# Kernel optimization log

Hardware: AMD Instinct MI355X
Metric: run time of the kernel (lower is better)

The kernel has to match this reference:

```python
import jax, jax.numpy as jnp
import numpy as np

HEADS = 6


def setup_inputs() -> dict:
    key = jax.random.key(0)
    ks = jax.random.split(key, 4)
    B, N, C = 4, 1024, 384
    s = 0.02
    return {
        "x": jax.random.normal(ks[0], (B, N, C), jnp.float32),
        "qkv_w": jax.random.normal(ks[1], (C, 3 * C), jnp.float32) * s,  # (in, out) layout
        "qkv_b": jnp.zeros((3 * C,), jnp.float32),
        "proj_w": jax.random.normal(ks[2], (C, C), jnp.float32) * s,
        "proj_b": jnp.zeros((C,), jnp.float32),
        "conv_w": jax.random.normal(ks[3], (HEADS, HEADS), jnp.float32) * s,  # 1x1 conv kernel (out_ch, in_ch)
        "conv_b": jnp.zeros((HEADS,), jnp.float32),
    }


def _forward(x, qkv_w, qkv_b, proj_w, proj_b, conv_w, conv_b):
    B, N, C = x.shape
    H = HEADS
    D = C // H
    scale = D ** -0.5
    qkv = (x @ qkv_w + qkv_b).reshape(B, N, 3, H, D)
    q = jnp.transpose(qkv[:, :, 0], (0, 2, 1, 3))  # bhnd
    k = jnp.transpose(qkv[:, :, 1], (0, 2, 1, 3))
    v = jnp.transpose(qkv[:, :, 2], (0, 2, 1, 3))
    qk = jnp.einsum('bhnd,bhmd->bhnm', q, k)          # raw scores (pre-scale)
    attn_mean = jax.nn.softmax(qk * scale, axis=-1)
    # data_uncertainty: 1x1 conv mixing the head channels of qk
    u = jnp.einsum('oh,bhnm->bonm', conv_w, qk) + conv_b[None, :, None, None]
    # norm_uncertainty: log(exp(u)) == u (kept faithful), then (tanh+1)/2
    u = jnp.log(jnp.exp(u))
    u = (jnp.tanh(u) + 1.0) * 0.5
    # gumbel-softmax (hard, tau=1) over logits [u, 1-u]; channel 1 selected.
    # softmax over 2 classes == sigmoid of logit difference; hard == argmax.
    gk = jax.random.key(42)
    g0 = jax.random.gumbel(jax.random.fold_in(gk, 0), u.shape, u.dtype)
    g1 = jax.random.gumbel(jax.random.fold_in(gk, 1), u.shape, u.dtype)
    l0 = u + g0
    l1 = (1.0 - u) + g1
    soft1 = jax.nn.sigmoid(l1 - l0)
    hard1 = (l1 > l0).astype(u.dtype)
    mask = hard1 + soft1 - jax.lax.stop_gradient(soft1)  # straight-through estimator
    attn = attn_mean * mask  # attn_drop is identity in eval / dropout=0
    out = jnp.einsum('bhnm,bhmd->bnhd', attn, v).reshape(B, N, C)
    out = out @ proj_w + proj_b  # proj_drop identity
    return out, attn_mean, u


def reference(x, qkv_w, qkv_b, proj_w, proj_b, conv_w, conv_b):
    return _forward(x, qkv_w, qkv_b, proj_w, proj_b, conv_w, conv_b)
```

## Files before the change

### kernel.cpp

```cpp
#include <hip/hip_runtime.h>
#include <hip/hip_bf16.h>
#include <stdint.h>
#include <stddef.h>

#define B_ 4
#define N_ 1024
#define C_ 384
#define H_ 6
#define D_ 64
#define TC_ 1152
#define BHNN_ 25165824
#define SCALE 0.125f
#define LOG2E 1.4426950408889634f
#define LN2 0.6931471805599453f

typedef __hip_bfloat16 bf16;
typedef __attribute__((ext_vector_type(2))) float f32x2;
typedef __attribute__((ext_vector_type(4))) float f32x4;
typedef __attribute__((ext_vector_type(8))) short short8;
typedef __attribute__((ext_vector_type(4))) short short4v;

union f4u { f32x4 v4; f32x2 v2[2]; };

__device__ __forceinline__ short f2bs(float x){
  bf16 b = __float2bfloat16(x);
  return *reinterpret_cast<short*>(&b);
}

__device__ __forceinline__ void pk_fma_ll(f32x2& c, f32x2 a, f32x2 b){
  asm("v_pk_fma_f32 %0, %1, %2, %0 op_sel:[0,0,0] op_sel_hi:[0,1,1]" : "+v"(c) : "v"(a), "v"(b));
}
__device__ __forceinline__ void pk_fma_hh(f32x2& c, f32x2 a, f32x2 b){
  asm("v_pk_fma_f32 %0, %1, %2, %0 op_sel:[1,0,0] op_sel_hi:[1,1,1]" : "+v"(c) : "v"(a), "v"(b));
}

#define TFR(x0,x1,r) { x0 += x1; x1 = ((x1)<<(r))|((x1)>>(32-(r))); x1 ^= x0; }

__host__ __device__ __forceinline__ void tf2x32(uint32_t k0, uint32_t k1,
                                                uint32_t& x0, uint32_t& x1){
  uint32_t k2 = k0 ^ k1 ^ 0x1BD11BDAu;
  x0 += k0; x1 += k1;
  TFR(x0,x1,13) TFR(x0,x1,15) TFR(x0,x1,26) TFR(x0,x1,6)
  x0 += k1; x1 += k2 + 1u;
  TFR(x0,x1,17) TFR(x0,x1,29) TFR(x0,x1,16) TFR(x0,x1,24)
  x0 += k2; x1 += k0 + 2u;
  TFR(x0,x1,13) TFR(x0,x1,15) TFR(x0,x1,26) TFR(x0,x1,6)
  x0 += k0; x1 += k1 + 3u;
  TFR(x0,x1,17) TFR(x0,x1,29) TFR(x0,x1,16) TFR(x0,x1,24)
  x0 += k1; x1 += k2 + 4u;
  TFR(x0,x1,13) TFR(x0,x1,15) TFR(x0,x1,26) TFR(x0,x1,6)
  x0 += k2; x1 += k0 + 5u;
}

__device__ __forceinline__ uint32_t rotl32(uint32_t x, uint32_t r){
#if __has_builtin(__builtin_amdgcn_alignbit)
  return __builtin_amdgcn_alignbit(x, x, 32u - r);
#else
  return (x << r) | (x >> (32u - r));
#endif
}

__device__ __forceinline__ void tf_dual(uint32_t j,
    uint32_t ak0, uint32_t ak1, uint32_t ak2,
    uint32_t bk0, uint32_t bk1, uint32_t bk2,
    float& fA, float& fB){
  uint32_t x0 = ak0, x1 = j + ak1;
  uint32_t y0 = bk0, y1 = j + bk1;
  #define DTFR(r) { x0 += x1; y0 += y1;               \
                    x1 = rotl32(x1,(r)); y1 = rotl32(y1,(r)); \
                    x1 ^= x0; y1 ^= y0; }
  DTFR(13) DTFR(15) DTFR(26) DTFR(6)
  x0 += ak1; x1 += ak2 + 1u;  y0 += bk1; y1 += bk2 + 1u;
  DTFR(17) DTFR(29) DTFR(16) DTFR(24)
  x0 += ak2; x1 += ak0 + 2u;  y0 += bk2; y1 += bk0 + 2u;
  DTFR(13) DTFR(15) DTFR(26) DTFR(6)
  x0 += ak0; x1 += ak1 + 3u;  y0 += bk0; y1 += bk1 + 3u;
  DTFR(17) DTFR(29) DTFR(16) DTFR(24)
  x0 += ak1; x1 += ak2 + 4u;  y0 += bk1; y1 += bk2 + 4u;
  DTFR(13) DTFR(15) DTFR(26) DTFR(6)
  x0 += ak2; x1 += ak0 + 5u;  y0 += bk2; y1 += bk0 + 5u;
  #undef DTFR
  uint32_t bitsA = x0 ^ x1;
  uint32_t bitsB = y0 ^ y1;
  fA = fmaxf(__uint_as_float((bitsA >> 9) | 0x3F800000u) - 1.0f, 1.1754943508222875e-38f);
  fB = fmaxf(__uint_as_float((bitsB >> 9) | 0x3F800000u) - 1.0f, 1.1754943508222875e-38f);
}

__global__ __launch_bounds__(256) void k_prep(const float* __restrict__ x,
                                              const float* __restrict__ w,
                                              short* __restrict__ xhi, short* __restrict__ xlo,
                                              short* __restrict__ wThi, short* __restrict__ wTlo){
  const int t = threadIdx.x;
  if (blockIdx.x < 432){
    const int kt = blockIdx.x % 12, nt = blockIdx.x / 12;
    __shared__ float T[32][33];
    const int col = t & 31, row8 = t >> 5;
    #pragma unroll
    for (int i = 0; i < 4; i++)
      T[row8 + i*8][col] = w[(size_t)(kt*32 + row8 + i*8)*TC_ + nt*32 + col];
    __syncthreads();
    #pragma unroll
    for (int i = 0; i < 4; i++){
      int n = nt*32 + row8 + i*8;
      int k = kt*32 + col;
      float v = T[col][row8 + i*8];
      bf16 hb = __float2bfloat16(v);
      float hf = __bfloat162float(hb);
      bf16 lb = __float2bfloat16(v - hf);
      wThi[(size_t)n*C_ + k] = *(short*)&hb;
      wTlo[(size_t)n*C_ + k] = *(short*)&lb;
    }
  } else {
    const int b2 = blockIdx.x - 432;
    size_t base = ((size_t)b2*256 + t) * 4;
    #pragma unroll
    for (int it = 0; it < 8; it++){
      size_t idx = base + (size_t)it * 196608;
      f32x4 v = *(const f32x4*)&x[idx];
      short4v hs, ls;
      #pragma unroll
      for (int jj = 0; jj < 4; jj++){
        bf16 hb = __float2bfloat16(v[jj]);
        float hf = __bfloat162float(hb);
        bf16 lb = __float2bfloat16(v[jj] - hf);
        hs[jj] = *(short*)&hb; ls[jj] = *(short*)&lb;
      }
      *(short4v*)&xhi[idx] = hs;
      *(short4v*)&xlo[idx] = ls;
    }
  }
}

__global__ __launch_bounds__(256) void k_qkv(const short* __restrict__ xhi,
                                             const short* __restrict__ xlo,
                                             const short* __restrict__ wThi,
                                             const short* __restrict__ wTlo,
                                             const float* __restrict__ bias,
                                             bf16* __restrict__ qb,
                                             bf16* __restrict__ kb,
                                             bf16* __restrict__ vTb){
  __shared__ __align__(16) short sA[2][64][32];
  __shared__ __align__(16) short sB[2][64][32];
  const int t = threadIdx.x, lane = t & 63, wv = t >> 6;
  const int lo = lane & 15, quad = lane >> 4;
  const int m0 = blockIdx.x * 64, n0 = blockIdx.y * 64;
  const int sr = lane >> 2, skq = lane & 3;
  const short* srcAh = xhi  + (size_t)(m0 + wv*16 + sr)*C_ + skq*8;
  const short* srcAl = xlo  + (size_t)(m0 + wv*16 + sr)*C_ + skq*8;
  const short* srcBh = wThi + (size_t)(n0 + wv*16 + sr)*C_ + skq*8;
  const short* srcBl = wTlo + (size_t)(n0 + wv*16 + sr)*C_ + skq*8;
  short* dAh = &sA[0][wv*16 + sr][skq*8];
  short* dAl = &sA[1][wv*16 + sr][skq*8];
  short* dBh = &sB[0][wv*16 + sr][skq*8];
  short* dBl = &sB[1][wv*16 + sr][skq*8];

  f32x4 acc[4] = {{0,0,0,0},{0,0,0,0},{0,0,0,0},{0,0,0,0}};
  short8 ra = *(const short8*)(srcAh);
  short8 rb = *(const short8*)(srcAl);
  short8 rc = *(const short8*)(srcBh);
  short8 rd = *(const short8*)(srcBl);
  for (int k0 = 0; k0 < C_; k0 += 32){
    __syncthreads();
    *(short8*)dAh = ra; *(short8*)dAl = rb;
    *(short8*)dBh = rc; *(short8*)dBl = rd;
    if (k0 + 32 < C_){
      ra = *(const short8*)(srcAh + k0 + 32);
      rb = *(const short8*)(srcAl + k0 + 32);
      rc = *(const short8*)(srcBh + k0 + 32);
      rd = *(const short8*)(srcBl + k0 + 32);
    }
    __syncthreads();
    short8 ah = *(const short8*)&sA[0][wv*16 + lo][quad*8];
    short8 al = *(const short8*)&sA[1][wv*16 + lo][quad*8];
    #pragma unroll
    for (int j = 0; j < 4; j++){
      short8 bh = *(const short8*)&sB[0][j*16 + lo][quad*8];
      short8 bl = *(const short8*)&sB[1][j*16 + lo][quad*8];
      acc[j] = __builtin_amdgcn_mfma_f32_16x16x32_bf16(ah, bh, acc[j], 0, 0, 0);
      acc[j] = __builtin_amdgcn_mfma_f32_16x16x32_bf16(ah, bl, acc[j], 0, 0, 0);
      acc[j] = __builtin_amdgcn_mfma_f32_16x16x32_bf16(al, bh, acc[j], 0, 0, 0);
    }
  }
  #pragma unroll
  for (int j = 0; j < 4; j++){
    int ng = n0 + j*16 + lo;
    int t3 = ng / C_;
    int rem = ng - t3*C_;
    int hh = rem >> 6, dd = rem & 63;
    float bsv = bias[ng];
    #pragma unroll
    for (int r = 0; r < 4; r++){
      int mg = m0 + wv*16 + quad*4 + r;
      int bb = mg >> 10, nn = mg & 1023;
      bf16 val = __float2bfloat16(acc[j][r] + bsv);
      if (t3 == 0)      qb[((size_t)(bb*H_ + hh)*N_ + nn)*D_ + dd] = val;
      else if (t3 == 1) kb[((size_t)(bb*H_ + hh)*N_ + nn)*D_ + dd] = val;
      else              vTb[((size_t)(bb*H_ + hh)*D_ + dd)*N_ + nn] = val;
    }
  }
}

__global__ __launch_bounds__(256) void k_scores(const short* __restrict__ qb,
                                                const short* __restrict__ kb,
                                                float* __restrict__ qk){
  const int gw = blockIdx.x * 4 + (threadIdx.x >> 6);
  const int lane = threadIdx.x & 63;
  const int mt = gw & 63, nt = (gw >> 6) & 63, bh = gw >> 12;
  const int lo = lane & 15, quad = lane >> 4;
  const short* qrow = qb + ((size_t)bh*N_ + nt*16 + lo)*D_ + quad*8;
  const short* krow = kb + ((size_t)bh*N_ + mt*16 + lo)*D_ + quad*8;
  short8 a0 = *(const short8*)qrow;
  short8 b0 = *(const short8*)krow;
  short8 a1 = *(const short8*)(qrow + 32);
  short8 b1 = *(const short8*)(krow + 32);
  f32x4 acc = {0.f, 0.f, 0.f, 0.f};
  acc = __builtin_amdgcn_mfma_f32_16x16x32_bf16(a0, b0, acc, 0, 0, 0);
  acc = __builtin_amdgcn_mfma_f32_16x16x32_bf16(a1, b1, acc, 0, 0, 0);
  float* o = qk + (size_t)bh*N_*N_ + (size_t)(nt*16)*N_ + mt*16;
  #pragma unroll
  for (int r = 0; r < 4; r++)
    o[(size_t)(quad*4 + r)*N_ + lo] = acc[r];
}

__global__ __launch_bounds__(256) void k_fuse(float* __restrict__ attn,
                                              const float* __restrict__ cw,
                                              const float* __restrict__ cb,
                                              float* __restrict__ u_out,
                                              unsigned long long* __restrict__ mbits,
                                              uint32_t g0k0, uint32_t g0k1,
                                              uint32_t g1k0, uint32_t g1k1){
  const int bn = blockIdx.x;
  const int bb = bn >> 10, n = bn & 1023;
  const int t = threadIdx.x, lane = t & 63, wid = t >> 6;
  __shared__ float redm[H_][4], reds[H_][4];

  float qv[H_][4];
  #pragma unroll
  for (int h = 0; h < H_; h++){
    const float* p = attn + (((size_t)(bb*H_ + h) << 10) + n) * N_;
    #pragma unroll
    for (int i = 0; i < 4; i++) qv[h][i] = p[t + 256*i];
  }
  #pragma unroll
  for (int h = 0; h < H_; h++){
    float mx = fmaxf(fmaxf(qv[h][0], qv[h][1]), fmaxf(qv[h][2], qv[h][3]));
    #pragma unroll
    for (int off = 32; off > 0; off >>= 1) mx = fmaxf(mx, __shfl_xor(mx, off));
    if (lane == 0) redm[h][wid] = mx;
  }
  __syncthreads();
  float mxh[H_], sm[H_];
  #pragma unroll
  for (int h = 0; h < H_; h++){
    mxh[h] = fmaxf(fmaxf(redm[h][0], redm[h][1]), fmaxf(redm[h][2], redm[h][3]));
    const float k2 = SCALE * LOG2E;
    float s = 0.f;
    #pragma unroll
    for (int i = 0; i < 4; i++) s += __builtin_amdgcn_exp2f((qv[h][i] - mxh[h]) * k2);
    #pragma unroll
    for (int off = 32; off > 0; off >>= 1) s += __shfl_xor(s, off);
    if (lane == 0) reds[h][wid] = s;
    sm[h] = s;
  }
  __syncthreads();
  float invS[H_];
  #pragma unroll
  for (int h = 0; h < H_; h++){
    float S = reds[h][0] + reds[h][1] + reds[h][2] + reds[h][3];
    invS[h] = __builtin_amdgcn_rcpf(S);
  }
  #pragma unroll
  for (int h = 0; h < H_; h++){
    float* p = attn + (((size_t)(bb*H_ + h) << 10) + n) * N_;
    const float k2 = SCALE * LOG2E;
    #pragma unroll
    for (int i = 0; i < 4; i++)
      p[t + 256*i] = __builtin_amdgcn_exp2f((qv[h][i] - mxh[h]) * k2) * invS[h];
  }
  const uint32_t a2k = g0k0 ^ g0k1 ^ 0x1BD11BDAu;
  const uint32_t b2k = g1k0 ^ g1k1 ^ 0x1BD11BDAu;
  const uint32_t jrow = ((uint32_t)(bb*H_) << 20) | ((uint32_t)n << 10);
  #pragma unroll
  for (int i = 0; i < 4; i++){
    const uint32_t m = (uint32_t)(t + 256*i);
    #pragma unroll
    for (int o = 0; o < H_; o++){
      float up = cb[o];
      #pragma unroll
      for (int h = 0; h < H_; h++) up += cw[o*H_ + h] * qv[h][i];
      float eneg = __builtin_amdgcn_exp2f(-2.0f * LOG2E * up);
      float uu   = __builtin_amdgcn_rcpf(1.0f + eneg);
      float tt   = 2.0f * uu - 1.0f;
      float et   = __builtin_amdgcn_exp2f(tt * LOG2E);
      uint32_t j = jrow + ((uint32_t)o << 20) + m;
      float f0, f1;
      tf_dual(j, g0k0, g0k1, a2k, g1k0, g1k1, b2k, f0, f1);
      float L0 = __builtin_amdgcn_logf(f0);
      float L1 = __builtin_amdgcn_logf(f1);
      int hard = L0 < L1 * et;
      u_out[(size_t)j] = uu;
      unsigned long long bal = __ballot(hard);
      if (lane == 0) mbits[(size_t)j >> 6] = bal;
    }
  }
}

__global__ __launch_bounds__(256) void k_av(const float* __restrict__ attn,
                                            const unsigned long long* __restrict__ mbits,
                                            const short* __restrict__ vTb,
                                            float* __restrict__ tmp){
  __shared__ __align__(16) float red[2][4][64][4];
  const int w = threadIdx.x >> 6, lane = threadIdx.x & 63;
  const int ntl = w >> 1, mh = w & 1;
  const int bh = blockIdx.x >> 5, ntp = blockIdx.x & 31;
  const int nt = ntp*2 + ntl;
  const int bb = bh / H_, h = bh - bb*H_;
  const int lo = lane & 15, quad = lane >> 4;
  const int row = nt*16 + lo;
  const float* arow = attn + ((size_t)bh*N_ + row)*N_ + quad*8;
  const unsigned long long* mrow = mbits + (((size_t)bh*N_ + row)*N_ >> 6);
  const short* vbase = vTb + ((size_t)bh*D_ + lo)*N_ + quad*8;
  f32x4 acc[4] = {{0,0,0,0},{0,0,0,0},{0,0,0,0},{0,0,0,0}};
  const int mstart = mh * 512;
  for (int m0 = mstart; m0 < mstart + 512; m0 += 32){
    f32x4 av0 = *(const f32x4*)(arow + m0);
    f32x4 av1 = *(const f32x4*)(arow + m0 + 4);
    unsigned long long wb = mrow[(m0 + quad*8) >> 6];
    int base = (m0 + quad*8) & 63;
    float vals[8] = {av0[0], av0[1], av0[2], av0[3], av1[0], av1[1], av1[2], av1[3]};
    short8 a;
    #pragma unroll
    for (int j = 0; j < 8; j++)
      a[j] = f2bs(((wb >> (base + j)) & 1ull) ? vals[j] : 0.0f);
    #pragma unroll
    for (int dt = 0; dt < 4; dt++){
      short8 bv = *(const short8*)(vbase + (size_t)(dt*16)*N_ + m0);
      acc[dt] = __builtin_amdgcn_mfma_f32_16x16x32_bf16(a, bv, acc[dt], 0, 0, 0);
    }
  }
  if (mh == 1){
    #pragma unroll
    for (int dt = 0; dt < 4; dt++)
      *(f32x4*)&red[ntl][dt][lane][0] = acc[dt];
  }
  __syncthreads();
  if (mh == 0){
    float* o = tmp + ((size_t)(bb*N_) + nt*16)*C_ + h*D_;
    #pragma unroll
    for (int dt = 0; dt < 4; dt++){
      f32x4 other = *(const f32x4*)&red[ntl][dt][lane][0];
      f32x4 s = acc[dt] + other;
      #pragma unroll
      for (int r = 0; r < 4; r++)
        o[(size_t)(quad*4 + r)*C_ + dt*16 + lo] = s[r];
    }
  }
}

__global__ __launch_bounds__(256) void k_proj(const float* __restrict__ A,
                                              const float* __restrict__ w,
                                              const float* __restrict__ bias,
                                              float* __restrict__ out){
  __shared__ __align__(16) float As[16][36];
  __shared__ __align__(16) float Bs[16][68];
  const int t = threadIdx.x, tx = t & 15, ty = t >> 4;
  const int m0 = blockIdx.x * 32, n0 = blockIdx.y * 64;
  const int am = t >> 3,        ak = (t & 7) * 2;
  const int bn = (t & 15) * 4,  bk = t >> 4;
  f32x2 c[2][2] = {};
  for (int k0 = 0; k0 < C_; k0 += 16){
    f32x2 av = *(const f32x2*)&A[(size_t)(m0+am)*C_ + k0 + ak];
    f32x4 bv = *(const f32x4*)&w[(size_t)(k0+bk)*C_ + n0 + bn];
    __syncthreads();
    As[ak+0][am] = av[0]; As[ak+1][am] = av[1];
    *(f32x4*)&Bs[bk][bn] = bv;
    __syncthreads();
    #pragma unroll
    for (int k = 0; k < 16; k++){
      f32x2 a2 = *(const f32x2*)&As[k][ty*2];
      f4u b; b.v4 = *(const f32x4*)&Bs[k][tx*4];
      pk_fma_ll(c[0][0], a2, b.v2[0]); pk_fma_ll(c[0][1], a2, b.v2[1]);
      pk_fma_hh(c[1][0], a2, b.v2[0]); pk_fma_hh(c[1][1], a2, b.v2[1]);
    }
  }
  #pragma unroll
  for (int i = 0; i < 2; i++)
    #pragma unroll
    for (int jp = 0; jp < 2; jp++)
      #pragma unroll
      for (int sub = 0; sub < 2; sub++){
        int jg = n0 + tx*4 + jp*2 + sub;
        out[(size_t)(m0+ty*2+i)*C_ + jg] = c[i][jp][sub] + bias[jg];
      }
}

extern "C" void kernel_launch(void* const* d_in, const int* in_sizes, int n_in,
                              void* d_out, int out_size, void* d_ws, size_t ws_size,
                              hipStream_t stream) {
  const float* x      = (const float*)d_in[0];
  const float* qkv_w  = (const float*)d_in[1];
  const float* qkv_b  = (const float*)d_in[2];
  const float* proj_w = (const float*)d_in[3];
  const float* proj_b = (const float*)d_in[4];
  const float* conv_w = (const float*)d_in[5];
  const float* conv_b = (const float*)d_in[6];

  float* out      = (float*)d_out;
  float* attn_out = out + (size_t)B_*N_*C_;
  float* u_out    = attn_out + (size_t)BHNN_;

  char* ws = (char*)d_ws;
  bf16*  qb    = (bf16*)ws;
  bf16*  kb    = (bf16*)(ws + 3145728);
  bf16*  vTb   = (bf16*)(ws + 6291456);
  unsigned long long* mbits = (unsigned long long*)(ws + 9437184);
  float* tmp   = (float*)(ws + 12582912);
  short* xhi   = (short*)(ws + 18874368);
  short* xlo   = (short*)(ws + 22020096);
  short* wThi  = (short*)(ws + 25165824);
  short* wTlo  = (short*)(ws + 26050560);

  uint32_t g0k0, g0k1, g1k0, g1k1;
  { uint32_t a = 0u, b = 0u; tf2x32(0u, 42u, a, b); g0k0 = a; g0k1 = b; }
  { uint32_t a = 0u, b = 1u; tf2x32(0u, 42u, a, b); g1k0 = a; g1k1 = b; }

  dim3 blk(256);
  k_prep  <<<dim3(624),     blk, 0, stream>>>(x, qkv_w, xhi, xlo, wThi, wTlo);
  k_qkv   <<<dim3(64, 18),  blk, 0, stream>>>(xhi, xlo, wThi, wTlo, qkv_b, qb, kb, vTb);
  k_scores<<<dim3(24576),   blk, 0, stream>>>((const short*)qb, (const short*)kb, attn_out);
  k_fuse  <<<dim3(4096),    blk, 0, stream>>>(attn_out, conv_w, conv_b,
                                              u_out, mbits,
                                              g0k0, g0k1, g1k0, g1k1);
  k_av    <<<dim3(768),     blk, 0, stream>>>(attn_out, mbits, (const short*)vTb, tmp);
  k_proj  <<<dim3(128, 6),  blk, 0, stream>>>(tmp, proj_w, proj_b, out);
}
```

Before: 436.1 us.

## Write masked bf16 attention in fuse kernel and swizzle GEMM block mapping

When the workspace is large enough, the fuse kernel writes the masked softmax probabilities directly as bf16. A new AV kernel then streams that bf16 matrix instead of re-reading fp32 attention plus mask bits, cutting AV read traffic roughly in half at the cost of an extra 50MB write. The QKV and projection GEMMs also remap their block indices so that blocks spread across XCDs share tiles, aiming for better L2 locality. The active path depends on the runtime workspace size.

```diff
diff --git a/kernel.cpp b/kernel.cpp
--- a/kernel.cpp
+++ b/kernel.cpp
@@ -143,7 +143,8 @@
   __shared__ __align__(16) short sB[2][64][32];
   const int t = threadIdx.x, lane = t & 63, wv = t >> 6;
   const int lo = lane & 15, quad = lane >> 4;
-  const int m0 = blockIdx.x * 64, n0 = blockIdx.y * 64;
+  const int wg = (blockIdx.x & 7) * 144 + (blockIdx.x >> 3);
+  const int m0 = (wg / 18) * 64, n0 = (wg % 18) * 64;
   const int sr = lane >> 2, skq = lane & 3;
   const short* srcAh = xhi  + (size_t)(m0 + wv*16 + sr)*C_ + skq*8;
   const short* srcAl = xlo  + (size_t)(m0 + wv*16 + sr)*C_ + skq*8;
@@ -222,11 +223,13 @@
     o[(size_t)(quad*4 + r)*N_ + lo] = acc[r];
 }
 
-__global__ __launch_bounds__(256) void k_fuse(float* __restrict__ attn,
+template<bool WRITE_AB>
+__global__ __launch_bounds__(256) void k_fuse_t(float* __restrict__ attn,
                                               const float* __restrict__ cw,
                                               const float* __restrict__ cb,
                                               float* __restrict__ u_out,
                                               unsigned long long* __restrict__ mbits,
+                                              bf16* __restrict__ ab,
                                               uint32_t g0k0, uint32_t g0k1,
                                               uint32_t g1k0, uint32_t g1k1){
   const int bn = blockIdx.x;
@@ -249,7 +252,7 @@
     if (lane == 0) redm[h][wid] = mx;
   }
   __syncthreads();
-  float mxh[H_], sm[H_];
+  float mxh[H_];
   #pragma unroll
   for (int h = 0; h < H_; h++){
     mxh[h] = fmaxf(fmaxf(redm[h][0], redm[h][1]), fmaxf(redm[h][2], redm[h][3]));
@@ -260,7 +263,6 @@
     #pragma unroll
     for (int off = 32; off > 0; off >>= 1) s += __shfl_xor(s, off);
     if (lane == 0) reds[h][wid] = s;
-    sm[h] = s;
   }
   __syncthreads();
   float invS[H_];
@@ -299,8 +301,15 @@
       float L1 = __builtin_amdgcn_logf(f1);
       int hard = L0 < L1 * et;
       u_out[(size_t)j] = uu;
-      unsigned long long bal = __ballot(hard);
-      if (lane == 0) mbits[(size_t)j >> 6] = bal;
+      if (WRITE_AB){
+        const float k2 = SCALE * LOG2E;
+        float e = __builtin_amdgcn_exp2f((qv[o][i] - mxh[o]) * k2) * invS[o];
+        bf16 mv = __float2bfloat16(hard ? e : 0.0f);
+        ab[(size_t)j] = mv;
+      } else {
+        unsigned long long bal = __ballot(hard);
+        if (lane == 0) mbits[(size_t)j >> 6] = bal;
+      }
     }
   }
 }
@@ -357,6 +366,48 @@
   }
 }
 
+__global__ __launch_bounds__(256) void k_av2(const short* __restrict__ ab,
+                                             const short* __restrict__ vTb,
+                                             float* __restrict__ tmp){
+  __shared__ __align__(16) float red[2][4][64][4];
+  const int w = threadIdx.x >> 6, lane = threadIdx.x & 63;
+  const int ntl = w >> 1, mh = w & 1;
+  const int bh = blockIdx.x >> 5, ntp = blockIdx.x & 31;
+  const int nt = ntp*2 + ntl;
+  const int bb = bh / H_, h = bh - bb*H_;
+  const int lo = lane & 15, quad = lane >> 4;
+  const int row = nt*16 + lo;
+  const short* abrow = ab + ((size_t)bh*N_ + row)*N_ + quad*8;
+  const short* vbase = vTb + ((size_t)bh*D_ + lo)*N_ + quad*8;
+  f32x4 acc[4] = {{0,0,0,0},{0,0,0,0},{0,0,0,0},{0,0,0,0}};
+  const int mstart = mh * 512;
+  for (int m0 = mstart; m0 < mstart + 512; m0 += 32){
+    short8 a = *(const short8*)(abrow + m0);
+    #pragma unroll
+    for (int dt = 0; dt < 4; dt++){
+      short8 bv = *(const short8*)(vbase + (size_t)(dt*16)*N_ + m0);
+      acc[dt] = __builtin_amdgcn_mfma_f32_16x16x32_bf16(a, bv, acc[dt], 0, 0, 0);
+    }
+  }
+  if (mh == 1){
+    #pragma unroll
+    for (int dt = 0; dt < 4; dt++)
+      *(f32x4*)&red[ntl][dt][lane][0] = acc[dt];
+  }
+  __syncthreads();
+  if (mh == 0){
+    float* o = tmp + ((size_t)(bb*N_) + nt*16)*C_ + h*D_;
+    #pragma unroll
+    for (int dt = 0; dt < 4; dt++){
+      f32x4 other = *(const f32x4*)&red[ntl][dt][lane][0];
+      f32x4 s = acc[dt] + other;
+      #pragma unroll
+      for (int r = 0; r < 4; r++)
+        o[(size_t)(quad*4 + r)*C_ + dt*16 + lo] = s[r];
+    }
+  }
+}
+
 __global__ __launch_bounds__(256) void k_proj(const float* __restrict__ A,
                                               const float* __restrict__ w,
                                               const float* __restrict__ bias,
@@ -364,7 +415,8 @@
   __shared__ __align__(16) float As[16][36];
   __shared__ __align__(16) float Bs[16][68];
   const int t = threadIdx.x, tx = t & 15, ty = t >> 4;
-  const int m0 = blockIdx.x * 32, n0 = blockIdx.y * 64;
+  const int wg = ((int)blockIdx.x & 7) * 96 + ((int)blockIdx.x >> 3);
+  const int m0 = (wg / 6) * 32, n0 = (wg % 6) * 64;
   const int am = t >> 3,        ak = (t & 7) * 2;
   const int bn = (t & 15) * 4,  bk = t >> 4;
   f32x2 c[2][2] = {};
@@ -419,6 +471,8 @@
   short* xlo   = (short*)(ws + 22020096);
   short* wThi  = (short*)(ws + 25165824);
   short* wTlo  = (short*)(ws + 26050560);
+  bf16*  ab    = (bf16*)(ws + 26935296);
+  const bool big_ws = ws_size >= (size_t)77266944;
 
   uint32_t g0k0, g0k1, g1k0, g1k1;
   { uint32_t a = 0u, b = 0u; tf2x32(0u, 42u, a, b); g0k0 = a; g0k1 = b; }
@@ -426,11 +480,18 @@
 
   dim3 blk(256);
   k_prep  <<<dim3(624),     blk, 0, stream>>>(x, qkv_w, xhi, xlo, wThi, wTlo);
-  k_qkv   <<<dim3(64, 18),  blk, 0, stream>>>(xhi, xlo, wThi, wTlo, qkv_b, qb, kb, vTb);
+  k_qkv   <<<dim3(1152),    blk, 0, stream>>>(xhi, xlo, wThi, wTlo, qkv_b, qb, kb, vTb);
   k_scores<<<dim3(24576),   blk, 0, stream>>>((const short*)qb, (const short*)kb, attn_out);
-  k_fuse  <<<dim3(4096),    blk, 0, stream>>>(attn_out, conv_w, conv_b,
-                                              u_out, mbits,
-                                              g0k0, g0k1, g1k0, g1k1);
-  k_av    <<<dim3(768),     blk, 0, stream>>>(attn_out, mbits, (const short*)vTb, tmp);
-  k_proj  <<<dim3(128, 6),  blk, 0, stream>>>(tmp, proj_w, proj_b, out);
-}
+  if (big_ws){
+    k_fuse_t<true> <<<dim3(4096), blk, 0, stream>>>(attn_out, conv_w, conv_b,
+                                                    u_out, mbits, ab,
+                                                    g0k0, g0k1, g1k0, g1k1);
+    k_av2 <<<dim3(768),     blk, 0, stream>>>((const short*)ab, (const short*)vTb, tmp);
+  } else {
+    k_fuse_t<false><<<dim3(4096), blk, 0, stream>>>(attn_out, conv_w, conv_b,
+                                                    u_out, mbits, ab,
+                                                    g0k0, g0k1, g1k0, g1k1);
+    k_av  <<<dim3(768),     blk, 0, stream>>>(attn_out, mbits, (const short*)vTb, tmp);
+  }
+  k_proj  <<<dim3(768),     blk, 0, stream>>>(tmp, proj_w, proj_b, out);
+}
```

Result: no change. 436.4 us (+0.1%).
